# Kernel optimization log

Measured on AMD Instinct MI355X. Metric: run time of the kernel, lower is better.

## Reference

```python
import jax, jax.numpy as jnp
import numpy as np

D = 768      # hidden_size
L = 4        # num_hidden_layers
H = 12       # num_attention_heads
I = 3072     # intermediate_size
B, S = 2, 2048
EPS = 1e-5


def setup_inputs() -> dict:
    key = jax.random.key(0)
    ks = jax.random.split(key, 8)
    sc = 0.02
    return {
        "x": jax.random.normal(ks[0], (B, S, D), dtype=jnp.float32),
        # weights stored as [in, out] so y = x @ W + b (same math as torch Linear)
        "qkv_w": jax.random.normal(ks[1], (L, D, 3 * D), dtype=jnp.float32) * sc,
        "qkv_b": jnp.zeros((L, 3 * D), dtype=jnp.float32),
        "out_w": jax.random.normal(ks[2], (L, D, D), dtype=jnp.float32) * sc,
        "out_b": jnp.zeros((L, D), dtype=jnp.float32),
        "ln1_w": jnp.ones((L, D), dtype=jnp.float32),
        "ln1_b": jnp.zeros((L, D), dtype=jnp.float32),
        "fc1_w": jax.random.normal(ks[3], (L, D, I), dtype=jnp.float32) * sc,
        "fc1_b": jnp.zeros((L, I), dtype=jnp.float32),
        "fc2_w": jax.random.normal(ks[4], (L, I, D), dtype=jnp.float32) * sc,
        "fc2_b": jnp.zeros((L, D), dtype=jnp.float32),
        "ln2_w": jnp.ones((L, D), dtype=jnp.float32),
        "ln2_b": jnp.zeros((L, D), dtype=jnp.float32),
    }


def _layer_norm(x, w, b):
    mu = jnp.mean(x, axis=-1, keepdims=True)
    var = jnp.mean(jnp.square(x - mu), axis=-1, keepdims=True)
    return (x - mu) * jax.lax.rsqrt(var + EPS) * w + b


def _encoder(x, qkv_w, qkv_b, out_w, out_b, ln1_w, ln1_b,
             fc1_w, fc1_b, fc2_w, fc2_b, ln2_w, ln2_b):
    hd = D // H
    scale = 1.0 / jnp.sqrt(jnp.float32(hd))

    def block(x, p):
        (qw, qb, ow, ob, l1w, l1b, f1w, f1b, f2w, f2b, l2w, l2b) = p
        # --- attention sub-block (pre-norm residual) ---
        h = _layer_norm(x, l1w, l1b)
        qkv = h @ qw + qb                      # [B,S,3D]
        qkv = qkv.reshape(B, S, H, 3 * hd).transpose(0, 2, 1, 3)  # [B,H,S,3hd]
        q, k, v = jnp.split(qkv, 3, axis=-1)
        logits = jnp.einsum('bhqd,bhkd->bhqk', q, k) * scale       # [B,H,S,S]
        attn = jax.nn.softmax(logits, axis=-1)
        vals = jnp.einsum('bhqk,bhkd->bhqd', attn, v)              # [B,H,S,hd]
        vals = vals.transpose(0, 2, 1, 3).reshape(B, S, D)
        x = x + vals @ ow + ob
        # --- MLP sub-block (pre-norm residual) ---
        h = _layer_norm(x, l2w, l2b)
        h = jax.nn.gelu(h @ f1w + f1b, approximate=False)
        x = x + h @ f2w + f2b
        return x, None

    params = (qkv_w, qkv_b, out_w, out_b, ln1_w, ln1_b,
              fc1_w, fc1_b, fc2_w, fc2_b, ln2_w, ln2_b)
    x, _ = jax.lax.scan(block, x, params)
    return x


def reference(x, qkv_w, qkv_b, out_w, out_b, ln1_w, ln1_b,
              fc1_w, fc1_b, fc2_w, fc2_b, ln2_w, ln2_b):
    return _encoder(x, qkv_w, qkv_b, out_w, out_b, ln1_w, ln1_b,
                    fc1_w, fc1_b, fc2_w, fc2_b, ln2_w, ln2_b)
```

## Files before the change

kernel.cpp:

```cpp
#include <hip/hip_runtime.h>
#include <stdint.h>
#include <math.h>

#define D_MODEL 768
#define NTOK    4096
#define SEQ     2048
#define NHEAD   12
#define HDIM    64
#define D_FF    3072
#define QKV_N   2304

typedef unsigned short ushort_t;
typedef short  short8 __attribute__((ext_vector_type(8)));
typedef float  f32x4  __attribute__((ext_vector_type(4)));
typedef float  f32x16 __attribute__((ext_vector_type(16)));

__device__ __forceinline__ float b2f(ushort_t u) {
  union { unsigned int u; float f; } v; v.u = ((unsigned int)u) << 16; return v.f;
}
__device__ __forceinline__ ushort_t f2b(float f) {
  union { float f; unsigned int u; } v; v.f = f;
  unsigned int u = v.u;
  return (ushort_t)((u + 0x7fffu + ((u >> 16) & 1u)) >> 16);
}
__device__ __forceinline__ unsigned cvtpk_bf16(float lo, float hi) {
  unsigned r;
  asm("v_cvt_pk_bf16_f32 %0, %1, %2" : "=v"(r) : "v"(lo), "v"(hi));
  return r;
}

__global__ __launch_bounds__(256) void transpose_layers(
    const float* __restrict__ qkv_w, const float* __restrict__ out_w,
    const float* __restrict__ fc1_w, const float* __restrict__ fc2_w,
    ushort_t* __restrict__ qkvT, ushort_t* __restrict__ outT,
    ushort_t* __restrict__ f1T, ushort_t* __restrict__ f2T) {
  __shared__ ushort_t tile[32][33];
  int bid = blockIdx.x;
  size_t l = blockIdx.y;
  const float* src; ushort_t* dst; int K, N, tn, tk;
  if (bid < 1728)      { src = qkv_w + l * D_MODEL * QKV_N; dst = qkvT + l * D_MODEL * QKV_N;
                         K = 768;  N = 2304; tn = bid % 72;  tk = bid / 72; }
  else if (bid < 2304) { int b = bid - 1728; src = out_w + l * D_MODEL * D_MODEL; dst = outT + l * D_MODEL * D_MODEL;
                         K = 768;  N = 768;  tn = b % 24; tk = b / 24; }
  else if (bid < 4608) { int b = bid - 2304; src = fc1_w + l * D_MODEL * D_FF; dst = f1T + l * D_MODEL * D_FF;
                         K = 768;  N = 3072; tn = b % 96; tk = b / 96; }
  else                 { int b = bid - 4608; src = fc2_w + l * D_FF * D_MODEL; dst = f2T + l * D_FF * D_MODEL;
                         K = 3072; N = 768;  tn = b % 24; tk = b / 24; }
  int n0 = tn * 32, k0 = tk * 32;
  int tx = threadIdx.x, ty = threadIdx.y;
  #pragma unroll
  for (int i = 0; i < 32; i += 8)
    tile[ty + i][tx] = f2b(src[(size_t)(k0 + ty + i) * N + n0 + tx]);
  __syncthreads();
  #pragma unroll
  for (int i = 0; i < 32; i += 8)
    dst[(size_t)(n0 + ty + i) * K + k0 + tx] = tile[tx][ty + i];
}

__global__ __launch_bounds__(256) void ln_kernel(const float* __restrict__ x,
                                                 const float* __restrict__ w,
                                                 const float* __restrict__ b,
                                                 ushort_t* __restrict__ out) {
  __shared__ float red[4];
  int tok = blockIdx.x, t = threadIdx.x;
  const float* xr = x + (size_t)tok * D_MODEL;
  float v0 = xr[t], v1 = xr[t + 256], v2 = xr[t + 512];
  float s = v0 + v1 + v2;
  #pragma unroll
  for (int o = 1; o < 64; o <<= 1) s += __shfl_xor(s, o, 64);
  if ((t & 63) == 0) red[t >> 6] = s;
  __syncthreads();
  float mean = (red[0] + red[1] + red[2] + red[3]) * (1.0f / 768.0f);
  __syncthreads();
  float d0 = v0 - mean, d1 = v1 - mean, d2 = v2 - mean;
  float q = d0 * d0 + d1 * d1 + d2 * d2;
  #pragma unroll
  for (int o = 1; o < 64; o <<= 1) q += __shfl_xor(q, o, 64);
  if ((t & 63) == 0) red[t >> 6] = q;
  __syncthreads();
  float var = (red[0] + red[1] + red[2] + red[3]) * (1.0f / 768.0f);
  float rs = rsqrtf(var + 1e-5f);
  ushort_t* orow = out + (size_t)tok * D_MODEL;
  orow[t]       = f2b(d0 * rs * w[t]       + b[t]);
  orow[t + 256] = f2b(d1 * rs * w[t + 256] + b[t + 256]);
  orow[t + 512] = f2b(d2 * rs * w[t + 512] + b[t + 512]);
}

template <int EPI, int TN>
__global__ __launch_bounds__(256) void gemm_kernel(
    const ushort_t* __restrict__ A, const ushort_t* __restrict__ BT,
    const float* __restrict__ bias, const float* __restrict__ resid,
    float* __restrict__ Cf, ushort_t* __restrict__ Cb, int M, int N, int K) {
  constexpr int NI = (TN == 128) ? 4 : 2;
  __shared__ ushort_t As[2][128 * 32];
  __shared__ ushort_t Bs[2][TN * 32];
  int t = threadIdx.x;
  int lane = t & 63, wave = t >> 6;
  int gx = gridDim.x;
  int nwg = gx * gridDim.y;
  int bid0 = blockIdx.y * gx + blockIdx.x;
  int qn = nwg >> 3, rm = nwg & 7;
  int xcd = bid0 & 7, pos = bid0 >> 3;
  int wg = (xcd < rm ? xcd * (qn + 1) : rm * (qn + 1) + (xcd - rm) * qn) + pos;
  int m0 = (wg / gx) * 128, n0 = (wg % gx) * TN;
  int wm = (TN == 128) ? (wave & 1) * 64 : wave * 32;
  int wn = (TN == 128) ? (wave >> 1) * 64 : 0;
  int quad = lane >> 4, l16 = lane & 15;
  int kq = quad * 8;
  int lrow = lane >> 2, lcol = (lane & 3) * 8;

  auto stage = [&](int k0, int buf) {
    #pragma unroll
    for (int c = 0; c < 2; ++c) {
      int rowA = wave * 32 + c * 16 + lrow;
      const ushort_t* ga = A + (size_t)(m0 + rowA) * K + k0 + lcol;
      ushort_t* la = &As[buf][(wave * 32 + c * 16) * 32];
      __builtin_amdgcn_global_load_lds((const __attribute__((address_space(1))) void*)ga,
                                       (__attribute__((address_space(3))) void*)la, 16, 0, 0);
      if (TN == 128 || c == 0) {
        int rowB = (TN == 128) ? rowA : (wave * 16 + lrow);
        const ushort_t* gb = BT + (size_t)(n0 + rowB) * K + k0 + lcol;
        ushort_t* lb = (TN == 128) ? &Bs[buf][(wave * 32 + c * 16) * 32]
                                   : &Bs[buf][(wave * 16) * 32];
        __builtin_amdgcn_global_load_lds((const __attribute__((address_space(1))) void*)gb,
                                         (__attribute__((address_space(3))) void*)lb, 16, 0, 0);
      }
    }
  };

  f32x4 acc[NI][4];
  #pragma unroll
  for (int i = 0; i < NI; ++i)
    #pragma unroll
    for (int j = 0; j < 4; ++j) acc[i][j] = (f32x4){0.f, 0.f, 0.f, 0.f};

  stage(0, 0);
  int nk = K / 32;
  for (int ki = 0; ki < nk; ++ki) {
    int cur = ki & 1;
    __syncthreads();
    if (ki + 1 < nk) stage((ki + 1) * 32, cur ^ 1);
    short8 af[NI], bf[4];
    #pragma unroll
    for (int i = 0; i < NI; ++i)
      af[i] = *(const short8*)&As[cur][(wm + i * 16 + l16) * 32 + kq];
    #pragma unroll
    for (int j = 0; j < 4; ++j)
      bf[j] = *(const short8*)&Bs[cur][(wn + j * 16 + l16) * 32 + kq];
    #pragma unroll
    for (int i = 0; i < NI; ++i)
      #pragma unroll
      for (int j = 0; j < 4; ++j)
        acc[i][j] = __builtin_amdgcn_mfma_f32_16x16x32_bf16(af[i], bf[j], acc[i][j], 0, 0, 0);
  }

  #pragma unroll
  for (int i = 0; i < NI; ++i) {
    #pragma unroll
    for (int j = 0; j < 4; ++j) {
      int col = n0 + wn + j * 16 + l16;
      float bv = bias[col];
      #pragma unroll
      for (int r = 0; r < 4; ++r) {
        int row = m0 + wm + i * 16 + quad * 4 + r;
        float v = acc[i][j][r] + bv;
        if (EPI == 1) {
          float u = v + 0.044715f * v * v * v;
          u = fminf(u, 30.0f);
          float e = exp2f(2.302207848f * u);
          v = v * e / (e + 1.0f);
        }
        if (EPI == 2) v += resid[(size_t)row * N + col];
        if (EPI == 2) Cf[(size_t)row * N + col] = v;
        else          Cb[(size_t)row * N + col] = f2b(v);
      }
    }
  }
}

__global__ __launch_bounds__(256, 3) void attn_kernel(const ushort_t* __restrict__ qkv,
                                                      ushort_t* __restrict__ out) {
  __shared__ __align__(16) ushort_t Ks[2][64 * 72];
  __shared__ __align__(16) ushort_t Vt[2][64 * 72];
  int t = threadIdx.x;
  int lane = t & 63, wave = t >> 6;
  int l31 = lane & 31, h = lane >> 5, h8 = h * 8;
  int kh = wave & 1, qh = wave >> 1;
  int kw = kh * 32;
  int qt = blockIdx.x;
  int bh = blockIdx.y;
  int b = bh / NHEAD, hd = bh % NHEAD;
  size_t base = (size_t)b * SEQ * QKV_N + hd * 192;

  const float kscale = 0.125f * 1.44269504088896f;

  short8 qf[4];
  {
    const ushort_t* qp = qkv + base + (size_t)(qt * 64 + qh * 32 + l31) * QKV_N + h8;
    #pragma unroll
    for (int ks = 0; ks < 4; ++ks) qf[ks] = *(const short8*)(qp + ks * 16);
  }

  int krow = t >> 1, kcol = (t & 1) * 32;
  int kcb = krow >> 6, krl = krow & 63;
  int kp = t & 63, vdb = (t >> 6) * 16;
  int vcb = kp >> 5, kpl = kp & 31;
  short8 kr[4], va[2], vb[2];
  auto kv_load = [&](int sbase) {
    const ushort_t* gk = qkv + base + (size_t)(sbase + krow) * QKV_N + 64 + kcol;
    #pragma unroll
    for (int i = 0; i < 4; ++i) kr[i] = *(const short8*)(gk + i * 8);
    const ushort_t* gv = qkv + base + (size_t)(sbase + 2 * kp) * QKV_N + 128 + vdb;
    va[0] = *(const short8*)gv;           va[1] = *(const short8*)(gv + 8);
    vb[0] = *(const short8*)(gv + QKV_N); vb[1] = *(const short8*)(gv + QKV_N + 8);
  };
  auto kv_write = [&]() {
    #pragma unroll
    for (int i = 0; i < 4; ++i)
      *(short8*)&Ks[kcb][krl * 72 + kcol + i * 8] = kr[i];
    unsigned* vtw = (unsigned*)&Vt[vcb][0];
    #pragma unroll
    for (int half = 0; half < 2; ++half)
      #pragma unroll
      for (int e = 0; e < 8; ++e) {
        unsigned pk = (unsigned)(unsigned short)va[half][e] |
                      ((unsigned)(unsigned short)vb[half][e] << 16);
        vtw[(vdb + half * 8 + e) * 36 + kpl] = pk;
      }
  };

  f32x16 o0, o1;
  #pragma unroll
  for (int i = 0; i < 16; ++i) { o0[i] = 0.f; o1[i] = 0.f; }
  float ls = 0.f;

  kv_load(0);
  for (int it = 0; it < SEQ / 128; ++it) {
    kv_write();
    __syncthreads();
    if (it + 1 < SEQ / 128) kv_load((it + 1) * 128);

    #pragma unroll
    for (int c = 0; c < 2; ++c) {
      f32x16 s;
      #pragma unroll
      for (int i = 0; i < 16; ++i) s[i] = 0.f;
      __builtin_amdgcn_s_setprio(1);
      #pragma unroll
      for (int ks = 0; ks < 4; ++ks) {
        short8 kf = *(const short8*)&Ks[c][(kw + l31) * 72 + ks * 16 + h8];
        s = __builtin_amdgcn_mfma_f32_32x32x16_bf16(kf, qf[ks], s, 0, 0, 0);
      }
      __builtin_amdgcn_s_setprio(0);

      unsigned wpk[4][2];
      #pragma unroll
      for (int g = 0; g < 4; ++g) {
        float p0 = exp2f(s[4 * g + 0] * kscale), p1 = exp2f(s[4 * g + 1] * kscale);
        float p2 = exp2f(s[4 * g + 2] * kscale), p3 = exp2f(s[4 * g + 3] * kscale);
        ls += (p0 + p1) + (p2 + p3);
        wpk[g][0] = cvtpk_bf16(p0, p1);
        wpk[g][1] = cvtpk_bf16(p2, p3);
      }

      #pragma unroll
      for (int k4 = 0; k4 < 2; ++k4) {
        int j2 = k4 * 2;
        unsigned f[4];
        #pragma unroll
        for (int c2 = 0; c2 < 2; ++c2) {
          unsigned a  = wpk[j2][c2];
          unsigned b2 = wpk[j2 + 1][c2];
          unsigned snd = h ? a : b2;
          unsigned rcv = (unsigned)__shfl_xor((int)snd, 32, 64);
          f[c2]     = h ? rcv : a;
          f[2 + c2] = h ? b2 : rcv;
        }
        union { unsigned u[4]; short8 s8; } uc;
        uc.u[0] = f[0]; uc.u[1] = f[1]; uc.u[2] = f[2]; uc.u[3] = f[3];
        short8 ap = uc.s8;
        short8 v0 = *(const short8*)&Vt[c][(l31)      * 72 + kw + k4 * 16 + h8];
        short8 v1 = *(const short8*)&Vt[c][(32 + l31) * 72 + kw + k4 * 16 + h8];
        __builtin_amdgcn_s_setprio(1);
        o0 = __builtin_amdgcn_mfma_f32_32x32x16_bf16(ap, v0, o0, 0, 0, 0);
        o1 = __builtin_amdgcn_mfma_f32_32x32x16_bf16(ap, v1, o1, 0, 0, 0);
        __builtin_amdgcn_s_setprio(0);
      }
    }
    __syncthreads();
  }

  float* slab = (float*)&Ks[0][0];
  if (kh == 1) {
    float* s = slab + (size_t)(qh * 64 + lane) * 33;
    #pragma unroll
    for (int i = 0; i < 16; ++i) { s[i] = o0[i]; s[16 + i] = o1[i]; }
    s[32] = ls;
  }
  __syncthreads();
  if (kh == 0) {
    float* s = slab + (size_t)(qh * 64 + lane) * 33;
    #pragma unroll
    for (int i = 0; i < 16; ++i) { o0[i] += s[i]; o1[i] += s[16 + i]; }
    ls += s[32];
    ls += __shfl_xor(ls, 32, 64);

    size_t ob = (size_t)(b * SEQ + qt * 64 + qh * 32) * D_MODEL + hd * HDIM;
    #pragma unroll
    for (int g = 0; g < 4; ++g) {
      #pragma unroll
      for (int r = 0; r < 4; ++r) {
        int reg = 4 * g + r;
        int qrow = 8 * g + 4 * h + r;
        float inv = 1.0f / __shfl(ls, qrow, 64);
        ushort_t* orow = out + ob + (size_t)qrow * D_MODEL;
        orow[l31]      = f2b(o0[reg] * inv);
        orow[32 + l31] = f2b(o1[reg] * inv);
      }
    }
  }
}

extern "C" void kernel_launch(void* const* d_in, const int* in_sizes, int n_in,
                              void* d_out, int out_size, void* d_ws, size_t ws_size,
                              hipStream_t stream) {
  const float* x_in  = (const float*)d_in[0];
  const float* qkv_w = (const float*)d_in[1];
  const float* qkv_b = (const float*)d_in[2];
  const float* out_w = (const float*)d_in[3];
  const float* out_b = (const float*)d_in[4];
  const float* ln1_w = (const float*)d_in[5];
  const float* ln1_b = (const float*)d_in[6];
  const float* fc1_w = (const float*)d_in[7];
  const float* fc1_b = (const float*)d_in[8];
  const float* fc2_w = (const float*)d_in[9];
  const float* fc2_b = (const float*)d_in[10];
  const float* ln2_w = (const float*)d_in[11];
  const float* ln2_b = (const float*)d_in[12];

  char* ws = (char*)d_ws;
  size_t off = 0;
  auto alloc = [&](size_t bytes) -> void* {
    void* p = ws + off; off += (bytes + 255) & ~(size_t)255; return p;
  };
  float*    buf_x  = (float*)   alloc((size_t)NTOK * D_MODEL * 4);
  float*    buf_x2 = (float*)   alloc((size_t)NTOK * D_MODEL * 4);
  ushort_t* bigb   = (ushort_t*)alloc((size_t)NTOK * D_FF * 2);
  ushort_t* h_b    = (ushort_t*)alloc((size_t)NTOK * D_MODEL * 2);
  ushort_t* at_b   = (ushort_t*)alloc((size_t)NTOK * D_MODEL * 2);

  size_t per_layer_w = ((size_t)QKV_N * D_MODEL + (size_t)D_MODEL * D_MODEL +
                        (size_t)D_FF * D_MODEL * 2) * 2;
  bool all_layers = (ws_size >= off + 4 * per_layer_w + (4 << 10));
  int nl = all_layers ? 4 : 1;
  ushort_t* qkvT = (ushort_t*)alloc((size_t)QKV_N * D_MODEL * 2 * nl);
  ushort_t* outT = (ushort_t*)alloc((size_t)D_MODEL * D_MODEL * 2 * nl);
  ushort_t* f1T  = (ushort_t*)alloc((size_t)D_FF * D_MODEL * 2 * nl);
  ushort_t* f2T  = (ushort_t*)alloc((size_t)D_MODEL * D_FF * 2 * nl);

  ushort_t* qkv_a = bigb;
  ushort_t* mlp_b = bigb;

  if (all_layers)
    transpose_layers<<<dim3(6912, 4), dim3(32, 8), 0, stream>>>(
        qkv_w, out_w, fc1_w, fc2_w, qkvT, outT, f1T, f2T);

  for (int l = 0; l < 4; ++l) {
    const float* resid_in = (l == 0) ? x_in : buf_x;
    size_t lw = all_layers ? (size_t)l : 0;
    ushort_t* qkvT_l = qkvT + lw * QKV_N * D_MODEL;
    ushort_t* outT_l = outT + lw * D_MODEL * D_MODEL;
    ushort_t* f1T_l  = f1T  + lw * D_FF * D_MODEL;
    ushort_t* f2T_l  = f2T  + lw * D_MODEL * D_FF;
    if (!all_layers)
      transpose_layers<<<dim3(6912, 1), dim3(32, 8), 0, stream>>>(
          qkv_w + (size_t)l * D_MODEL * QKV_N, out_w + (size_t)l * D_MODEL * D_MODEL,
          fc1_w + (size_t)l * D_MODEL * D_FF,  fc2_w + (size_t)l * D_FF * D_MODEL,
          qkvT_l, outT_l, f1T_l, f2T_l);
    ln_kernel<<<NTOK, 256, 0, stream>>>(resid_in, ln1_w + l * D_MODEL, ln1_b + l * D_MODEL, h_b);
    gemm_kernel<0, 128><<<dim3(QKV_N / 128, NTOK / 128), 256, 0, stream>>>(
        h_b, qkvT_l, qkv_b + l * QKV_N, nullptr, nullptr, qkv_a, NTOK, QKV_N, D_MODEL);
    attn_kernel<<<dim3(SEQ / 64, 2 * NHEAD), 256, 0, stream>>>(qkv_a, at_b);
    gemm_kernel<2, 64><<<dim3(D_MODEL / 64, NTOK / 128), 256, 0, stream>>>(
        at_b, outT_l, out_b + l * D_MODEL, resid_in, buf_x2, nullptr, NTOK, D_MODEL, D_MODEL);
    ln_kernel<<<NTOK, 256, 0, stream>>>(buf_x2, ln2_w + l * D_MODEL, ln2_b + l * D_MODEL, h_b);
    gemm_kernel<1, 128><<<dim3(D_FF / 128, NTOK / 128), 256, 0, stream>>>(
        h_b, f1T_l, fc1_b + l * D_FF, nullptr, nullptr, mlp_b, NTOK, D_FF, D_MODEL);
    float* x_next = (l < 3) ? buf_x : (float*)d_out;
    gemm_kernel<2, 64><<<dim3(D_MODEL / 64, NTOK / 128), 256, 0, stream>>>(
        mlp_b, f2T_l, fc2_b + l * D_MODEL, buf_x2, x_next, nullptr, NTOK, D_MODEL, D_FF);
  }
  (void)in_sizes; (void)n_in; (void)out_size;
}
```

Before: 943.6 us.

## Split attention key chunks across twice as many waves per block

The attention kernel now runs 8 waves per block instead of 4. Each wave handles one of the two 64-key chunks per iteration rather than looping over both, and the K/V staging loads are spread over the larger thread count. Partial outputs and row sums are merged with a two-stage shared-memory reduction. The aim is more parallelism and latency hiding inside the softmax and MFMA loop, at the cost of extra barriers and reduction traffic and a higher launch-bounds occupancy target that may pressure registers.

```diff
diff --git a/kernel.cpp b/kernel.cpp
--- a/kernel.cpp
+++ b/kernel.cpp
@@ -178,14 +178,16 @@
   }
 }
 
-__global__ __launch_bounds__(256, 3) void attn_kernel(const ushort_t* __restrict__ qkv,
+__global__ __launch_bounds__(512, 6) void attn_kernel(const ushort_t* __restrict__ qkv,
                                                       ushort_t* __restrict__ out) {
-  __shared__ __align__(16) ushort_t Ks[2][64 * 72];
-  __shared__ __align__(16) ushort_t Vt[2][64 * 72];
+  __shared__ __align__(16) ushort_t smem[4 * 64 * 72];
+  ushort_t* Ks = smem;
+  ushort_t* Vt = smem + 2 * 64 * 72;
   int t = threadIdx.x;
   int lane = t & 63, wave = t >> 6;
   int l31 = lane & 31, h = lane >> 5, h8 = h * 8;
-  int kh = wave & 1, qh = wave >> 1;
+  int c  = wave & 1;
+  int kh = (wave >> 1) & 1, qh = wave >> 2;
   int kw = kh * 32;
   int qt = blockIdx.x;
   int bh = blockIdx.y;
@@ -201,38 +203,38 @@
     for (int ks = 0; ks < 4; ++ks) qf[ks] = *(const short8*)(qp + ks * 16);
   }
 
-  int krow = t >> 1, kcol = (t & 1) * 32;
+  int krow = t >> 2, kcol = (t & 3) * 16;
   int kcb = krow >> 6, krl = krow & 63;
-  int kp = t & 63, vdb = (t >> 6) * 16;
+  int kp = t & 63, vdb = (t >> 6) * 8;
   int vcb = kp >> 5, kpl = kp & 31;
-  short8 kr[4], va[2], vb[2];
+  short8 kr[2], va, vb;
   auto kv_load = [&](int sbase) {
     const ushort_t* gk = qkv + base + (size_t)(sbase + krow) * QKV_N + 64 + kcol;
-    #pragma unroll
-    for (int i = 0; i < 4; ++i) kr[i] = *(const short8*)(gk + i * 8);
+    kr[0] = *(const short8*)gk;
+    kr[1] = *(const short8*)(gk + 8);
     const ushort_t* gv = qkv + base + (size_t)(sbase + 2 * kp) * QKV_N + 128 + vdb;
-    va[0] = *(const short8*)gv;           va[1] = *(const short8*)(gv + 8);
-    vb[0] = *(const short8*)(gv + QKV_N); vb[1] = *(const short8*)(gv + QKV_N + 8);
+    va = *(const short8*)gv;
+    vb = *(const short8*)(gv + QKV_N);
   };
   auto kv_write = [&]() {
-    #pragma unroll
-    for (int i = 0; i < 4; ++i)
-      *(short8*)&Ks[kcb][krl * 72 + kcol + i * 8] = kr[i];
-    unsigned* vtw = (unsigned*)&Vt[vcb][0];
-    #pragma unroll
-    for (int half = 0; half < 2; ++half)
-      #pragma unroll
-      for (int e = 0; e < 8; ++e) {
-        unsigned pk = (unsigned)(unsigned short)va[half][e] |
-                      ((unsigned)(unsigned short)vb[half][e] << 16);
-        vtw[(vdb + half * 8 + e) * 36 + kpl] = pk;
-      }
+    *(short8*)&Ks[kcb * 4608 + krl * 72 + kcol]     = kr[0];
+    *(short8*)&Ks[kcb * 4608 + krl * 72 + kcol + 8] = kr[1];
+    unsigned* vtw = (unsigned*)&Vt[vcb * 4608];
+    #pragma unroll
+    for (int e = 0; e < 8; ++e) {
+      unsigned pk = (unsigned)(unsigned short)va[e] |
+                    ((unsigned)(unsigned short)vb[e] << 16);
+      vtw[(vdb + e) * 36 + kpl] = pk;
+    }
   };
 
   f32x16 o0, o1;
   #pragma unroll
   for (int i = 0; i < 16; ++i) { o0[i] = 0.f; o1[i] = 0.f; }
   float ls = 0.f;
+
+  const ushort_t* Ksc = Ks + c * 4608;
+  const ushort_t* Vtc = Vt + c * 4608;
 
   kv_load(0);
   for (int it = 0; it < SEQ / 128; ++it) {
@@ -240,69 +242,80 @@
     __syncthreads();
     if (it + 1 < SEQ / 128) kv_load((it + 1) * 128);
 
-    #pragma unroll
-    for (int c = 0; c < 2; ++c) {
-      f32x16 s;
+    f32x16 s;
+    #pragma unroll
+    for (int i = 0; i < 16; ++i) s[i] = 0.f;
+    __builtin_amdgcn_s_setprio(1);
+    #pragma unroll
+    for (int ks = 0; ks < 4; ++ks) {
+      short8 kf = *(const short8*)&Ksc[(kw + l31) * 72 + ks * 16 + h8];
+      s = __builtin_amdgcn_mfma_f32_32x32x16_bf16(kf, qf[ks], s, 0, 0, 0);
+    }
+    __builtin_amdgcn_s_setprio(0);
+
+    unsigned wpk[4][2];
+    #pragma unroll
+    for (int g = 0; g < 4; ++g) {
+      float p0 = exp2f(s[4 * g + 0] * kscale), p1 = exp2f(s[4 * g + 1] * kscale);
+      float p2 = exp2f(s[4 * g + 2] * kscale), p3 = exp2f(s[4 * g + 3] * kscale);
+      ls += (p0 + p1) + (p2 + p3);
+      wpk[g][0] = cvtpk_bf16(p0, p1);
+      wpk[g][1] = cvtpk_bf16(p2, p3);
+    }
+
+    #pragma unroll
+    for (int k4 = 0; k4 < 2; ++k4) {
+      int j2 = k4 * 2;
+      unsigned f[4];
       #pragma unroll
-      for (int i = 0; i < 16; ++i) s[i] = 0.f;
+      for (int c2 = 0; c2 < 2; ++c2) {
+        unsigned a  = wpk[j2][c2];
+        unsigned b2 = wpk[j2 + 1][c2];
+        unsigned snd = h ? a : b2;
+        unsigned rcv = (unsigned)__shfl_xor((int)snd, 32, 64);
+        f[c2]     = h ? rcv : a;
+        f[2 + c2] = h ? b2 : rcv;
+      }
+      union { unsigned u[4]; short8 s8; } uc;
+      uc.u[0] = f[0]; uc.u[1] = f[1]; uc.u[2] = f[2]; uc.u[3] = f[3];
+      short8 ap = uc.s8;
+      short8 v0 = *(const short8*)&Vtc[(l31)      * 72 + kw + k4 * 16 + h8];
+      short8 v1 = *(const short8*)&Vtc[(32 + l31) * 72 + kw + k4 * 16 + h8];
       __builtin_amdgcn_s_setprio(1);
-      #pragma unroll
-      for (int ks = 0; ks < 4; ++ks) {
-        short8 kf = *(const short8*)&Ks[c][(kw + l31) * 72 + ks * 16 + h8];
-        s = __builtin_amdgcn_mfma_f32_32x32x16_bf16(kf, qf[ks], s, 0, 0, 0);
-      }
+      o0 = __builtin_amdgcn_mfma_f32_32x32x16_bf16(ap, v0, o0, 0, 0, 0);
+      o1 = __builtin_amdgcn_mfma_f32_32x32x16_bf16(ap, v1, o1, 0, 0, 0);
       __builtin_amdgcn_s_setprio(0);
-
-      unsigned wpk[4][2];
-      #pragma unroll
-      for (int g = 0; g < 4; ++g) {
-        float p0 = exp2f(s[4 * g + 0] * kscale), p1 = exp2f(s[4 * g + 1] * kscale);
-        float p2 = exp2f(s[4 * g + 2] * kscale), p3 = exp2f(s[4 * g + 3] * kscale);
-        ls += (p0 + p1) + (p2 + p3);
-        wpk[g][0] = cvtpk_bf16(p0, p1);
-        wpk[g][1] = cvtpk_bf16(p2, p3);
-      }
-
-      #pragma unroll
-      for (int k4 = 0; k4 < 2; ++k4) {
-        int j2 = k4 * 2;
-        unsigned f[4];
-        #pragma unroll
-        for (int c2 = 0; c2 < 2; ++c2) {
-          unsigned a  = wpk[j2][c2];
-          unsigned b2 = wpk[j2 + 1][c2];
-          unsigned snd = h ? a : b2;
-          unsigned rcv = (unsigned)__shfl_xor((int)snd, 32, 64);
-          f[c2]     = h ? rcv : a;
-          f[2 + c2] = h ? b2 : rcv;
-        }
-        union { unsigned u[4]; short8 s8; } uc;
-        uc.u[0] = f[0]; uc.u[1] = f[1]; uc.u[2] = f[2]; uc.u[3] = f[3];
-        short8 ap = uc.s8;
-        short8 v0 = *(const short8*)&Vt[c][(l31)      * 72 + kw + k4 * 16 + h8];
-        short8 v1 = *(const short8*)&Vt[c][(32 + l31) * 72 + kw + k4 * 16 + h8];
-        __builtin_amdgcn_s_setprio(1);
-        o0 = __builtin_amdgcn_mfma_f32_32x32x16_bf16(ap, v0, o0, 0, 0, 0);
-        o1 = __builtin_amdgcn_mfma_f32_32x32x16_bf16(ap, v1, o1, 0, 0, 0);
-        __builtin_amdgcn_s_setprio(0);
-      }
     }
     __syncthreads();
   }
 
-  float* slab = (float*)&Ks[0][0];
-  if (kh == 1) {
-    float* s = slab + (size_t)(qh * 64 + lane) * 33;
-    #pragma unroll
-    for (int i = 0; i < 16; ++i) { s[i] = o0[i]; s[16 + i] = o1[i]; }
-    s[32] = ls;
-  }
-  __syncthreads();
-  if (kh == 0) {
-    float* s = slab + (size_t)(qh * 64 + lane) * 33;
-    #pragma unroll
-    for (int i = 0; i < 16; ++i) { o0[i] += s[i]; o1[i] += s[16 + i]; }
-    ls += s[32];
+  float* slab = (float*)smem;
+  if (c == 1) {
+    float* sp = slab + (size_t)((wave >> 1) * 64 + lane) * 33;
+    #pragma unroll
+    for (int i = 0; i < 16; ++i) { sp[i] = o0[i]; sp[16 + i] = o1[i]; }
+    sp[32] = ls;
+  }
+  __syncthreads();
+  if (c == 0) {
+    float* sp = slab + (size_t)((wave >> 1) * 64 + lane) * 33;
+    #pragma unroll
+    for (int i = 0; i < 16; ++i) { o0[i] += sp[i]; o1[i] += sp[16 + i]; }
+    ls += sp[32];
+  }
+  __syncthreads();
+  if (c == 0 && kh == 1) {
+    float* sp = slab + (size_t)(qh * 64 + lane) * 33;
+    #pragma unroll
+    for (int i = 0; i < 16; ++i) { sp[i] = o0[i]; sp[16 + i] = o1[i]; }
+    sp[32] = ls;
+  }
+  __syncthreads();
+  if (c == 0 && kh == 0) {
+    float* sp = slab + (size_t)(qh * 64 + lane) * 33;
+    #pragma unroll
+    for (int i = 0; i < 16; ++i) { o0[i] += sp[i]; o1[i] += sp[16 + i]; }
+    ls += sp[32];
     ls += __shfl_xor(ls, 32, 64);
 
     size_t ob = (size_t)(b * SEQ + qt * 64 + qh * 32) * D_MODEL + hd * HDIM;
@@ -380,7 +393,7 @@
     ln_kernel<<<NTOK, 256, 0, stream>>>(resid_in, ln1_w + l * D_MODEL, ln1_b + l * D_MODEL, h_b);
     gemm_kernel<0, 128><<<dim3(QKV_N / 128, NTOK / 128), 256, 0, stream>>>(
         h_b, qkvT_l, qkv_b + l * QKV_N, nullptr, nullptr, qkv_a, NTOK, QKV_N, D_MODEL);
-    attn_kernel<<<dim3(SEQ / 64, 2 * NHEAD), 256, 0, stream>>>(qkv_a, at_b);
+    attn_kernel<<<dim3(SEQ / 64, 2 * NHEAD), 512, 0, stream>>>(qkv_a, at_b);
     gemm_kernel<2, 64><<<dim3(D_MODEL / 64, NTOK / 128), 256, 0, stream>>>(
         at_b, outT_l, out_b + l * D_MODEL, resid_in, buf_x2, nullptr, NTOK, D_MODEL, D_MODEL);
     ln_kernel<<<NTOK, 256, 0, stream>>>(buf_x2, ln2_w + l * D_MODEL, ln2_b + l * D_MODEL, h_b);
```

Result: slower. 1.323 ms (+40.2%).
